# Optimization experiments

Hardware: AMD Instinct MI355X
Metric: run time of the kernel (lower is better)

Reference implementation:

```python
import jax, jax.numpy as jnp
import numpy as np

EPS = 1e-08
KERNEL = 3


def setup_inputs() -> dict:
    key = jax.random.key(0)
    k1, k2, k3, k4 = jax.random.split(key, 4)
    N, IN_CH, OUT_CH, H, W, STYLE_DIM = 16, 256, 256, 64, 64, 512
    x = jax.random.normal(k1, (N, IN_CH, H, W), dtype=jnp.float32)
    style = jax.random.normal(k2, (N, STYLE_DIM), dtype=jnp.float32)
    # base weight: [1, out_ch, in_ch, k, k] (torch.randn init)
    weight = jax.random.normal(k3, (1, OUT_CH, IN_CH, KERNEL, KERNEL), dtype=jnp.float32)
    # modulation Linear(style_dim -> in_ch): weight ~ N(0,1), bias = 0
    mod_w = jax.random.normal(k4, (IN_CH, STYLE_DIM), dtype=jnp.float32)
    mod_b = jnp.zeros((IN_CH,), dtype=jnp.float32)
    return {"x": x, "style": style, "weight": weight, "mod_w": mod_w, "mod_b": mod_b}


def _per_sample_conv(xi, wi):
    # xi: [in_ch, H, W], wi: [out_ch, in_ch, k, k]
    pad = KERNEL // 2
    out = jax.lax.conv_general_dilated(
        xi[None], wi,
        window_strides=(1, 1),
        padding=[(pad, pad), (pad, pad)],
        dimension_numbers=("NCHW", "OIHW", "NCHW"),
    )
    return out[0]  # [out_ch, H, W]


def reference(x, style, weight, mod_w, mod_b):
    # modulation: Linear(style) -> [N, in_ch]
    s = style @ mod_w.T + mod_b  # [N, in_ch]
    # modulate base weight: [N, out_ch, in_ch, k, k]
    w = weight * (s[:, None, :, None, None] + 1.0)
    # demodulate
    demod = jax.lax.rsqrt(jnp.sum(w * w, axis=(2, 3, 4)) + EPS)  # [N, out_ch]
    w = w * demod[:, :, None, None, None]
    # grouped conv with groups=N == per-sample conv, vmapped over batch
    out = jax.vmap(_per_sample_conv)(x, w)  # [N, out_ch, H, W]
    return out
```

## Files before the change

kernel.cpp:

```cpp
#include <hip/hip_runtime.h>
#include <hip/hip_bf16.h>
#include <stdint.h>


#define NB  16
#define IC  256
#define OC  256
#define HW  64
#define HWP 66
#define SD  512
#define SPATIAL 4096
#define HWPIC 16896

typedef __hip_bfloat16 bf16;
typedef __bf16 bf16x8 __attribute__((ext_vector_type(8)));
typedef float  f32x4  __attribute__((ext_vector_type(4)));
typedef uint32_t u32a3 __attribute__((address_space(3)));
typedef const uint32_t u32a1 __attribute__((address_space(1)));

static __device__ __forceinline__ unsigned short f2bu(float f) {
    bf16 h = __float2bfloat16(f);
    union { bf16 b; unsigned short u; } c; c.b = h; return c.u;
}
static __device__ __forceinline__ void gll16(const void* g, void* l) {
    __builtin_amdgcn_global_load_lds((u32a1*)g, (u32a3*)l, 16, 0, 0);
}

__global__ __launch_bounds__(256)
void k_prep1(const float* __restrict__ weight, const float* __restrict__ style,
             const float* __restrict__ mod_w, const float* __restrict__ mod_b,
             float* __restrict__ wsq, bf16* __restrict__ wt2,
             uint4* __restrict__ xs4, float* __restrict__ scale) {
    int b = blockIdx.x, t = threadIdx.x;
    if (b < 256) {
        int tid = b * 256 + t;
        const float* wp = weight + (size_t)tid * 9;
        float v[9], s = 0.f;
        #pragma unroll
        for (int r = 0; r < 9; ++r) { v[r] = wp[r]; s += v[r] * v[r]; }
        wsq[tid] = s;
        #pragma unroll
        for (int r = 0; r < 9; ++r) wt2[(r << 16) + tid] = __float2bfloat16(v[r]);
    } else if (b < 784) {
        int idx = b - 256;
        int n = idx / 33, bx = idx - n * 33;
        int f = bx * 256 + t;
        int u = f >> 5, q = f & 31;
        if (u >= 260) return;
        int rb;
        if      (u <  66) rb = u;
        else if (u < 132) rb = 65 * 66 + (u - 66);
        else if (u < 196) rb = (u - 131) * 66;
        else              rb = (u - 195) * 66 + 65;
        xs4[(size_t)n * 139392 + rb * 32 + q] = make_uint4(0u, 0u, 0u, 0u);
    } else {
        int lane = t & 63;
        int w = (b - 784) * 4 + (t >> 6);
        int n = w >> 8, ic = w & 255;
        const float4* mw4 = (const float4*)mod_w + (size_t)ic * 128 + lane * 2;
        const float4* st4 = (const float4*)style + (size_t)n * 128 + lane * 2;
        float4 a0 = mw4[0], a1 = mw4[1], s0 = st4[0], s1 = st4[1];
        float acc = a0.x*s0.x + a0.y*s0.y + a0.z*s0.z + a0.w*s0.w
                  + a1.x*s1.x + a1.y*s1.y + a1.z*s1.z + a1.w*s1.w;
        #pragma unroll
        for (int off = 32; off > 0; off >>= 1) acc += __shfl_down(acc, off);
        if (lane == 0) scale[w] = acc + mod_b[ic] + 1.0f;
    }
}

__global__ __launch_bounds__(256)
void k_prep2(const float* __restrict__ x, const float* __restrict__ scale,
             const float* __restrict__ wsq, bf16* __restrict__ xs,
             float* __restrict__ demod) {
    __shared__ unsigned short tile[HW * 256];
    int b = blockIdx.x, t = threadIdx.x;
    if (b < 1024) {
        int y = b & 63, n = b >> 6;
        const float* sc = scale + n * IC;
        const float4* xp4 = (const float4*)(x + ((size_t)n * IC) * SPATIAL + (size_t)y * HW);
        #pragma unroll
        for (int i = 0; i < 16; ++i) {
            int fid = i * 256 + t;
            int ic = fid >> 4, f4 = fid & 15;
            float4 v = xp4[(size_t)ic * 1024 + f4];
            float s = sc[ic];
            int sp = f4 << 2;
            int sw = ic ^ ((f4 & 7) << 3);
            tile[(sp + 0) * 256 + sw] = f2bu(v.x * s);
            tile[(sp + 1) * 256 + sw] = f2bu(v.y * s);
            tile[(sp + 2) * 256 + sw] = f2bu(v.z * s);
            tile[(sp + 3) * 256 + sw] = f2bu(v.w * s);
        }
        __syncthreads();
        uint4* dst4 = (uint4*)(xs + (((size_t)n * HWP + (y + 1)) * HWP + 1) * IC);
        #pragma unroll
        for (int j = 0; j < 8; ++j) {
            int uid = j * 256 + t;
            int sp = uid >> 5, g = uid & 31;
            dst4[sp * 32 + g] =
                *(const uint4*)&tile[sp * 256 + ((g ^ ((sp >> 2) & 7)) << 3)];
        }
    } else {
        int n = b - 1024, oc = t;
        float* sc = (float*)tile;
        sc[t] = scale[n * IC + t];
        __syncthreads();
        const float4* wp4 = (const float4*)(wsq + (size_t)oc * IC);
        const float4* sc4 = (const float4*)sc;
        float acc = 0.f;
        #pragma unroll 8
        for (int i = 0; i < 64; ++i) {
            float4 q = wp4[i], s = sc4[i];
            acc += q.x*s.x*s.x + q.y*s.y*s.y + q.z*s.z*s.z + q.w*s.w*s.w;
        }
        demod[n * OC + oc] = rsqrtf(acc + 1e-8f);
    }
}

#define VM6 asm volatile("s_waitcnt vmcnt(6)" ::: "memory")
#define BAR __builtin_amdgcn_s_barrier()

__global__ __launch_bounds__(512, 2)
void k_conv(const bf16* __restrict__ xs, const bf16* __restrict__ wt2,
            const float* __restrict__ demod, float* __restrict__ out) {
    extern __shared__ char smem[];
    int t = threadIdx.x, l = t & 63, w = t >> 6;
    int wm = w & 1, wn = w >> 1;
    int bid = blockIdx.x;
    int work = ((bid & 7) << 5) | (bid >> 3);
    int nimg = work >> 4;
    int ybase = (work & 15) << 2;
    int spb = (work & 15) << 8;

    int srow = (w << 3) + (l >> 3);
    int gseg = (l & 7) ^ (l >> 3);
    const bf16* gA = xs + (((size_t)nimg * HWP + ybase) * HWP + srow) * IC + (gseg << 3);
    const bf16* gB = wt2 + ((size_t)srow << 8) + (gseg << 3);
    int stW = w << 10;

    int aRow = ((wm << 6) + (l & 15)) << 7;
    int bRow = ((wn << 5) + (l & 15)) << 7;
    int sg0 = ((l >> 4) ^ (l & 7)) << 4;
    int sg1 = sg0 ^ 64;

    f32x4 acc[4][4][2];
    #pragma unroll
    for (int p = 0; p < 4; ++p)
        #pragma unroll
        for (int m = 0; m < 4; ++m)
            #pragma unroll
            for (int n = 0; n < 2; ++n) acc[p][m][n] = (f32x4){0.f, 0.f, 0.f, 0.f};

    bf16x8 af[4][2], bf0[2][2], bf1[2][2];

#define STG_A(ha, PARN, AOFF) do {                                          \
    const bf16* s_ = gA + (AOFF) + (ha) * 2 * HWPIC;                        \
    char* d_ = smem + (PARN) * 32768 + (ha) * 16384 + stW;                  \
    gll16(s_, d_); gll16(s_ + HWPIC, d_ + 8192); } while (0)
#define STG_B(hb, PARN, BOFF) do {                                          \
    const bf16* s_ = gB + (BOFF) + (hb) * (128 * IC);                       \
    char* d_ = smem + 65536 + (PARN) * 32768 + (hb) * 16384 + stW;          \
    gll16(s_, d_); gll16(s_ + 64 * IC, d_ + 8192); } while (0)
#define LD_A(QA) do { const char* Ab_ = Ap + (QA) * 16384 + aRow;           \
    _Pragma("unroll") for (int m_ = 0; m_ < 4; ++m_) {                      \
        af[m_][0] = *(const bf16x8*)(Ab_ + m_ * 2048 + sg0);                \
        af[m_][1] = *(const bf16x8*)(Ab_ + m_ * 2048 + sg1); } } while (0)
#define LD_B(DST, QB) do { const char* Bb_ = Bp + (QB) * 16384 + bRow;      \
    _Pragma("unroll") for (int n_ = 0; n_ < 2; ++n_) {                      \
        DST[n_][0] = *(const bf16x8*)(Bb_ + n_ * 2048 + sg0);               \
        DST[n_][1] = *(const bf16x8*)(Bb_ + n_ * 2048 + sg1); } } while (0)
#define MM(P, BF) do {                                                      \
    __builtin_amdgcn_s_setprio(1);                                          \
    _Pragma("unroll") for (int kk_ = 0; kk_ < 2; ++kk_)                     \
    _Pragma("unroll") for (int m_ = 0; m_ < 4; ++m_)                        \
    _Pragma("unroll") for (int n_ = 0; n_ < 2; ++n_)                        \
        acc[P][m_][n_] = __builtin_amdgcn_mfma_f32_16x16x32_bf16(           \
            af[m_][kk_], BF[n_][kk_], acc[P][m_][n_], 0, 0, 0);             \
    __builtin_amdgcn_s_setprio(0); } while (0)

    STG_A(0, 0, 0);
    STG_B(0, 0, 0);
    STG_B(1, 0, 0);
    STG_A(1, 0, 0);
    STG_A(0, 1, 64);
    VM6;
    BAR;

    #pragma clang loop unroll(disable)
    for (int T = 0; T < 36; ++T) {
        int par = T & 1, parn = par ^ 1;
        const char* Ap = smem + par * 32768;
        const char* Bp = smem + 65536 + par * 32768;
        int T1 = T + 1, T2 = T + 2;
        int r1 = T1 >> 2, ic1 = (T1 & 3) << 6;
        int ky1 = r1 / 3, kx1 = r1 - ky1 * 3;
        int aoff1 = T1 < 36 ? (ky1 * HWP + kx1) * IC + ic1 : 0;
        int boff1 = T1 < 36 ? (r1 << 16) + ic1 : 0;
        int r2 = T2 >> 2, ic2 = (T2 & 3) << 6;
        int ky2 = r2 / 3, kx2 = r2 - ky2 * 3;
        int aoff2 = T2 < 36 ? (ky2 * HWP + kx2) * IC + ic2 : 0;

        LD_A(0); LD_B(bf0, 0);
        STG_B(0, parn, boff1);
        VM6; BAR; MM(0, bf0);
        LD_B(bf1, 1);
        STG_B(1, parn, boff1);
        VM6; BAR; MM(1, bf1);
        LD_A(1);
        STG_A(1, parn, aoff1);
        BAR; MM(2, bf1);
        STG_A(0, par, aoff2);
        VM6; BAR; MM(3, bf0);
    }

    const float* dm = demod + nimg * OC;
    int ocol = l & 15, orow = (l >> 4) << 2;
    #pragma unroll
    for (int p = 0; p < 4; ++p) {
        int qa = p >> 1, qb = qa ^ (p & 1);
        #pragma unroll
        for (int n = 0; n < 2; ++n) {
            int oc = (qb << 7) + (wn << 5) + (n << 4) + ocol;
            float d = dm[oc];
            size_t ob = ((size_t)(nimg * OC + oc)) * SPATIAL
                      + spb + (qa << 7) + (wm << 6) + orow;
            #pragma unroll
            for (int m = 0; m < 4; ++m) {
                f32x4 a = acc[p][m][n];
                f32x4 o = { a[0] * d, a[1] * d, a[2] * d, a[3] * d };
                *reinterpret_cast<f32x4*>(out + ob + m * 16) = o;
            }
        }
    }
}

extern "C" void kernel_launch(void* const* d_in, const int* in_sizes, int n_in,
                              void* d_out, int out_size, void* d_ws, size_t ws_size,
                              hipStream_t stream) {
    const float* x      = (const float*)d_in[0];
    const float* style  = (const float*)d_in[1];
    const float* weight = (const float*)d_in[2];
    const float* mod_w  = (const float*)d_in[3];
    const float* mod_b  = (const float*)d_in[4];
    float* out = (float*)d_out;

    char* ws = (char*)d_ws;
    float* scale = (float*)(ws + 0);
    float* demod = (float*)(ws + 16384);
    float* wsq   = (float*)(ws + 32768);
    bf16*  wt2   = (bf16*)(ws + 294912);
    bf16*  xs    = (bf16*)(ws + 1474560);

    static int s_attr = 0;
    if (!s_attr) {
        hipFuncSetAttribute(reinterpret_cast<const void*>(k_conv),
                            hipFuncAttributeMaxDynamicSharedMemorySize, 131072);
        s_attr = 1;
    }

    k_prep1<<<1808, 256, 0, stream>>>(weight, style, mod_w, mod_b,
                                      wsq, wt2, (uint4*)xs, scale);
    k_prep2<<<1040, 256, 0, stream>>>(x, scale, wsq, xs, demod);
    k_conv<<<256, 512, 131072, stream>>>(xs, wt2, demod, out);
}
```

Before: 189.1 us.

## Restructure conv main loop with register double-buffered fragments and prefetch across tiles

Rewrites the K-loop of the implicit-GEMM conv so LDS fragment reads for the next tile (A half 0 and B half 0) happen at the end of the current tile. It uses ping-pong register sets (afA/afB, bf0A/bf0B) and sched_barriers to keep reads ahead of the MFMAs. The loop is unrolled by two with an explicit epilogue, and global-to-LDS staging is reordered with adjusted vmcnt waits. The aim is to hide LDS read latency behind MFMA work and cut stalls at barriers. In exchange it raises register pressure at 2 blocks per CU and makes the wait counts delicate.

Result: no change. 188.7 us (-0.2%).

```diff
diff --git a/kernel.cpp b/kernel.cpp
--- a/kernel.cpp
+++ b/kernel.cpp
@@ -117,8 +117,11 @@
     }
 }
 
-#define VM6 asm volatile("s_waitcnt vmcnt(6)" ::: "memory")
+#define VM4 asm volatile("s_waitcnt vmcnt(4)" ::: "memory")
+#define VM2 asm volatile("s_waitcnt vmcnt(2)" ::: "memory")
+#define VM0 asm volatile("s_waitcnt vmcnt(0)" ::: "memory")
 #define BAR __builtin_amdgcn_s_barrier()
+#define SB0 __builtin_amdgcn_sched_barrier(0)
 
 __global__ __launch_bounds__(512, 2)
 void k_conv(const bf16* __restrict__ xs, const bf16* __restrict__ wt2,
@@ -151,7 +154,7 @@
             #pragma unroll
             for (int n = 0; n < 2; ++n) acc[p][m][n] = (f32x4){0.f, 0.f, 0.f, 0.f};
 
-    bf16x8 af[4][2], bf0[2][2], bf1[2][2];
+    bf16x8 afA[4][2], afB[4][2], bf0A[2][2], bf0B[2][2], bf1[2][2];
 
 #define STG_A(ha, PARN, AOFF) do {                                          \
     const bf16* s_ = gA + (AOFF) + (ha) * 2 * HWPIC;                        \
@@ -161,56 +164,91 @@
     const bf16* s_ = gB + (BOFF) + (hb) * (128 * IC);                       \
     char* d_ = smem + 65536 + (PARN) * 32768 + (hb) * 16384 + stW;          \
     gll16(s_, d_); gll16(s_ + 64 * IC, d_ + 8192); } while (0)
-#define LD_A(QA) do { const char* Ab_ = Ap + (QA) * 16384 + aRow;           \
+#define RD_A(DST, BASE) do { const char* A_ = (const char*)(BASE);          \
     _Pragma("unroll") for (int m_ = 0; m_ < 4; ++m_) {                      \
-        af[m_][0] = *(const bf16x8*)(Ab_ + m_ * 2048 + sg0);                \
-        af[m_][1] = *(const bf16x8*)(Ab_ + m_ * 2048 + sg1); } } while (0)
-#define LD_B(DST, QB) do { const char* Bb_ = Bp + (QB) * 16384 + bRow;      \
+        DST[m_][0] = *(const bf16x8*)(A_ + m_ * 2048 + sg0);                \
+        DST[m_][1] = *(const bf16x8*)(A_ + m_ * 2048 + sg1); } } while (0)
+#define RD_B(DST, BASE) do { const char* B_ = (const char*)(BASE);          \
     _Pragma("unroll") for (int n_ = 0; n_ < 2; ++n_) {                      \
-        DST[n_][0] = *(const bf16x8*)(Bb_ + n_ * 2048 + sg0);               \
-        DST[n_][1] = *(const bf16x8*)(Bb_ + n_ * 2048 + sg1); } } while (0)
-#define MM(P, BF) do {                                                      \
+        DST[n_][0] = *(const bf16x8*)(B_ + n_ * 2048 + sg0);                \
+        DST[n_][1] = *(const bf16x8*)(B_ + n_ * 2048 + sg1); } } while (0)
+#define MM(P, AF, BF) do {                                                  \
     __builtin_amdgcn_s_setprio(1);                                          \
     _Pragma("unroll") for (int kk_ = 0; kk_ < 2; ++kk_)                     \
     _Pragma("unroll") for (int m_ = 0; m_ < 4; ++m_)                        \
     _Pragma("unroll") for (int n_ = 0; n_ < 2; ++n_)                        \
         acc[P][m_][n_] = __builtin_amdgcn_mfma_f32_16x16x32_bf16(           \
-            af[m_][kk_], BF[n_][kk_], acc[P][m_][n_], 0, 0, 0);             \
+            AF[m_][kk_], BF[n_][kk_], acc[P][m_][n_], 0, 0, 0);             \
     __builtin_amdgcn_s_setprio(0); } while (0)
+
+#define TILE(PAR, BF0C, BF0N, AOFF1, BOFF1) do {                            \
+    const char* Ap_  = smem + (PAR) * 32768;                                \
+    const char* Bp_  = smem + 65536 + (PAR) * 32768;                        \
+    const char* Apn_ = smem + ((PAR) ^ 1) * 32768;                          \
+    const char* Bpn_ = smem + 65536 + ((PAR) ^ 1) * 32768;                  \
+     \
+    STG_A(0, (PAR) ^ 1, AOFF1);                                             \
+    VM4; BAR;                                                               \
+    RD_B(bf1, Bp_ + 16384 + bRow);                                          \
+    SB0;                                                                    \
+    MM(0, afA, BF0C);                                                       \
+                        \
+    STG_B(0, (PAR) ^ 1, BOFF1);                                             \
+    VM4; BAR;                                                               \
+    RD_A(afB, Ap_ + 16384 + aRow);                                          \
+    SB0;                                                                    \
+    MM(1, afA, bf1);                                                        \
+                                               \
+    STG_B(1, (PAR) ^ 1, BOFF1);                                             \
+    BAR;                                                                    \
+    MM(2, afB, bf1);                                                        \
+            \
+    STG_A(1, (PAR) ^ 1, AOFF1);                                             \
+    VM4; BAR;                                                               \
+    RD_A(afA, Apn_ + aRow);                                                 \
+    RD_B(BF0N, Bpn_ + bRow);                                                \
+    SB0;                                                                    \
+    MM(3, afB, BF0C);                                                       \
+} while (0)
 
     STG_A(0, 0, 0);
     STG_B(0, 0, 0);
     STG_B(1, 0, 0);
     STG_A(1, 0, 0);
-    STG_A(0, 1, 64);
-    VM6;
+    VM4;
     BAR;
+    RD_A(afA, smem + aRow);
+    RD_B(bf0A, smem + 65536 + bRow);
 
     #pragma clang loop unroll(disable)
-    for (int T = 0; T < 36; ++T) {
-        int par = T & 1, parn = par ^ 1;
-        const char* Ap = smem + par * 32768;
-        const char* Bp = smem + 65536 + par * 32768;
-        int T1 = T + 1, T2 = T + 2;
-        int r1 = T1 >> 2, ic1 = (T1 & 3) << 6;
+    for (int TT = 0; TT < 17; ++TT) {
+        int Tn1 = 2 * TT + 1, Tn2 = 2 * TT + 2;
+        int r1 = Tn1 >> 2, ic1 = (Tn1 & 3) << 6;
         int ky1 = r1 / 3, kx1 = r1 - ky1 * 3;
-        int aoff1 = T1 < 36 ? (ky1 * HWP + kx1) * IC + ic1 : 0;
-        int boff1 = T1 < 36 ? (r1 << 16) + ic1 : 0;
-        int r2 = T2 >> 2, ic2 = (T2 & 3) << 6;
+        int aoff1 = (ky1 * HWP + kx1) * IC + ic1, boff1 = (r1 << 16) + ic1;
+        int r2 = Tn2 >> 2, ic2 = (Tn2 & 3) << 6;
         int ky2 = r2 / 3, kx2 = r2 - ky2 * 3;
-        int aoff2 = T2 < 36 ? (ky2 * HWP + kx2) * IC + ic2 : 0;
-
-        LD_A(0); LD_B(bf0, 0);
-        STG_B(0, parn, boff1);
-        VM6; BAR; MM(0, bf0);
-        LD_B(bf1, 1);
-        STG_B(1, parn, boff1);
-        VM6; BAR; MM(1, bf1);
-        LD_A(1);
-        STG_A(1, parn, aoff1);
-        BAR; MM(2, bf1);
-        STG_A(0, par, aoff2);
-        VM6; BAR; MM(3, bf0);
+        int aoff2 = (ky2 * HWP + kx2) * IC + ic2, boff2 = (r2 << 16) + ic2;
+        TILE(0, bf0A, bf0B, aoff1, boff1);
+        TILE(1, bf0B, bf0A, aoff2, boff2);
+    }
+    {
+        int aoff35 = (2 * HWP + 2) * IC + 192, boff35 = (8 << 16) + 192;
+        TILE(0, bf0A, bf0B, aoff35, boff35);
+    }
+    {
+        const char* Ap_ = smem + 32768;
+        const char* Bp_ = smem + 65536 + 32768;
+        VM2; BAR;
+        RD_B(bf1, Bp_ + 16384 + bRow);
+        SB0;
+        MM(0, afA, bf0B);
+        VM0; BAR;
+        RD_A(afB, Ap_ + 16384 + aRow);
+        SB0;
+        MM(1, afA, bf1);
+        MM(2, afB, bf1);
+        MM(3, afB, bf0B);
     }
 
     const float* dm = demod + nimg * OC;
```
